# Performance work log

Measured on AMD Instinct MI355X. Metric: run time of the kernel, lower is better.

The kernel has to match this reference:

```python
import jax, jax.numpy as jnp
import numpy as np

CHUNK_SIZE = 256


def setup_inputs() -> dict:
    key = jax.random.key(0)
    kq, kk, kv = jax.random.split(key, 3)
    b, h, L, d, dv = 2, 16, 4096, 16, 64
    return {
        "q": jax.random.normal(kq, (b, h, L, d), dtype=jnp.float32),
        "k": jax.random.normal(kk, (b, h, L, d), dtype=jnp.float32),
        "v": jax.random.normal(kv, (b, h, L, dv), dtype=jnp.float32),
    }


def reference(q, k, v):
    b, h, L, d = q.shape
    dv = v.shape[-1]
    cs = CHUNK_SIZE
    n = L // cs

    q = q * d ** (-0.5)

    # ---- normalizer z over full sequence ----
    k_cumsum = jnp.cumsum(k, axis=-2)                               # [b,h,L,d]
    kk_cumsum = jnp.cumsum(k[..., :, None] * k[..., None, :], axis=-3)  # [b,h,L,d,d]
    z = (q * k_cumsum).sum(-1)
    z = z + 0.5 * jnp.einsum('bhld,bhle,bhlde->bhl', q, q, kk_cumsum)
    z = z + (jnp.arange(L, dtype=z.dtype) + 1.0)[None, None, :]

    # ---- zeroth-order term ----
    o_const = jnp.cumsum(v, axis=-2)                                # [b,h,L,dv]

    # ---- chunked view ----
    qc = q.reshape(b, h, n, cs, d)
    kc = k.reshape(b, h, n, cs, d)
    vc = v.reshape(b, h, n, cs, dv)

    # intra-chunk quadratic attention: S + 0.5*S^2, causal-masked
    s = jnp.einsum('bhnqd,bhnkd->bhnqk', qc, kc)                    # [b,h,n,cs,cs]
    s = s + 0.5 * s ** 2
    causal_mask = jnp.tril(jnp.ones((cs, cs), dtype=bool))
    s = jnp.where(causal_mask, s, jnp.zeros((), dtype=s.dtype))
    o = jnp.einsum('bhnqk,bhnkf->bhnqf', s, vc)                     # [b,h,n,cs,dv]

    # inter-chunk quadratic state: cumulative K x K x V from previous chunks
    kv_quad = jnp.einsum('bhncd,bhnce,bhncf->bhndef', kc, kc, vc)   # [b,h,n,d,d,dv]
    kv_quad = jnp.cumsum(kv_quad, axis=2)
    kv_quad = jnp.concatenate(
        [jnp.zeros_like(kv_quad[:, :, :1]), kv_quad[:, :, :-1]], axis=2)
    o = o + 0.5 * jnp.einsum('bhndef,bhncd,bhnce->bhncf', kv_quad, qc, qc)

    # inter-chunk linear state: cumulative K x V from previous chunks
    kv_lin = jnp.einsum('bhncd,bhnce->bhnde', kc, vc)               # [b,h,n,d,dv]
    kv_lin = jnp.cumsum(kv_lin, axis=2)
    kv_lin = jnp.concatenate(
        [jnp.zeros_like(kv_lin[:, :, :1]), kv_lin[:, :, :-1]], axis=2)
    o = o + jnp.einsum('bhnde,bhncd->bhnce', kv_lin, qc)

    o = o.reshape(b, h, L, dv) + o_const
    return o / (z[..., None] + 1e-6)
```

## Files before the change

kernel.cpp:

```cpp
#include <hip/hip_runtime.h>
#include <hip/hip_cooperative_groups.h>
#include <cstddef>

#define BH    32
#define LSEQ  4096
#define D     16
#define DV    64
#define CS    256
#define NC    16
#define NF    160
#define NZ    65
#define KSTEPS 5
#define PER   (NZ * NF)
#define QXS   20

typedef short short8 __attribute__((ext_vector_type(8)));
typedef float f32x4 __attribute__((ext_vector_type(4)));
typedef float f4 __attribute__((ext_vector_type(4)));
typedef unsigned uint4v __attribute__((ext_vector_type(4)));

#define OFF_KBF 0u
#define OFF_VT  (4u*1024u*1024u)
#define OFF_ST  (OFF_VT + (unsigned)(BH*NZ*LSEQ*2))

__device__ __forceinline__ unsigned f2bf(float x) {
  unsigned u = __float_as_uint(x);
  return (u + 0x7FFFu + ((u >> 16) & 1u)) >> 16;
}
__device__ __forceinline__ float bf2f(unsigned short u) {
  return __uint_as_float(((unsigned)u) << 16);
}
__device__ __forceinline__ short8 zero8() {
  short8 z = {0,0,0,0,0,0,0,0};
  return z;
}
__device__ __forceinline__ unsigned cvtpk(float lo, float hi) {
  unsigned r;
  asm("v_cvt_pk_bf16_f32 %0, %1, %2" : "=v"(r) : "v"(lo), "v"(hi));
  return r;
}
__device__ __forceinline__ short8 pk4(unsigned a, unsigned b, unsigned c, unsigned d) {
  uint4v u = {a, b, c, d};
  return __builtin_bit_cast(short8, u);
}

__device__ __forceinline__ unsigned feat_tbl(int f) {
  if (f == 0)  return 16u | (16u << 8);
  if (f <= 16) return (unsigned)(f - 1) | (16u << 8);
  if (f < 137) {
    int p = f - 17, off = 0;
    for (int d = 0; d < 15; ++d) {
      int cnt = 15 - d;
      if (p < off + cnt) return (unsigned)d | ((unsigned)(d + 1 + p - off) << 8);
      off += cnt;
    }
  }
  if (f < 153) {
    int d = f - 137;
    return (unsigned)d | ((unsigned)d << 8) | (1u << 16);
  }
  return 17u | (17u << 8);
}

struct Smem {
  float kxqx[CS][QXS];
  __align__(16) unsigned short vt[NZ][264];
  union {
    __align__(16) unsigned short stt[NZ][168];
    struct {
      __align__(16) unsigned short ptile[8][1280];
      float zline[CS];
    } u;
  } b;
  unsigned tbl[NF];
};

__global__ __launch_bounds__(512, 4) void unified(const float* __restrict__ q,
                                                  const float* __restrict__ k,
                                                  const float* __restrict__ v,
                                                  unsigned* __restrict__ kbf_u32,
                                                  unsigned short* __restrict__ st,
                                                  float* __restrict__ out) {
  __shared__ Smem sm;
  int blk = blockIdx.x, bh = blk >> 4, c = blk & 15;
  int t = threadIdx.x, w = t >> 6, lane = t & 63, quad = lane >> 4, n16 = lane & 15;
  const size_t base = (size_t)bh * LSEQ + (size_t)c * CS;

  {
    const f4* K4 = (const f4*)(k + base * D);
    uint2* kbd2 = (uint2*)(kbf_u32 + base * D / 2);
    for (int idx = t; idx < 1024; idx += 512) {
      f4 kv = K4[idx];
      kbd2[idx] = make_uint2(cvtpk(kv[0], kv[1]), cvtpk(kv[2], kv[3]));
      *(f4*)&sm.kxqx[idx >> 2][(idx & 3) * 4] = kv;
    }
    for (int i = t; i < CS; i += 512)
      *(float2*)&sm.kxqx[i][16] = make_float2(1.f, 0.f);
    const f4* V4 = (const f4*)(v + base * DV);
    for (int idx = t; idx < 2048; idx += 512) {
      int m16 = idx & 15, j0 = (idx >> 4) * 2;
      f4 a  = V4[j0 * 16 + m16];
      f4 bq = V4[j0 * 16 + 16 + m16];
#pragma unroll
      for (int r = 0; r < 4; ++r)
        *(unsigned*)&sm.vt[m16 * 4 + r][j0] = cvtpk(a[r], bq[r]);
    }
    if (t < 128) ((unsigned*)&sm.vt[64][0])[t] = 0x3F803F80u;
    if (t < NF) sm.tbl[t] = feat_tbl(t);
  }
  __syncthreads();

  if (c < 15 && w < 5) {
    unsigned tv0 = sm.tbl[(w * 2 + 0) * 16 + n16];
    unsigned tv1 = sm.tbl[(w * 2 + 1) * 16 + n16];
    int d0 = tv0 & 255, e0 = (tv0 >> 8) & 255;
    int d1 = tv1 & 255, e1 = (tv1 >> 8) & 255;
    f32x4 acc[2][5];
#pragma unroll
    for (int mm = 0; mm < 2; ++mm)
#pragma unroll
      for (int nt = 0; nt < 5; ++nt) acc[mm][nt] = (f32x4){0.f, 0.f, 0.f, 0.f};
    for (int jt = 0; jt < 8; ++jt) {
      float x0[8], x1[8];
#pragma unroll
      for (int i = 0; i < 8; ++i) {
        const float* kr = &sm.kxqx[jt * 32 + quad * 8 + i][0];
        x0[i] = kr[d0] * kr[e0];
        x1[i] = kr[d1] * kr[e1];
      }
      short8 afr0 = pk4(cvtpk(x0[0], x0[1]), cvtpk(x0[2], x0[3]),
                        cvtpk(x0[4], x0[5]), cvtpk(x0[6], x0[7]));
      short8 afr1 = pk4(cvtpk(x1[0], x1[1]), cvtpk(x1[2], x1[3]),
                        cvtpk(x1[4], x1[5]), cvtpk(x1[6], x1[7]));
      __builtin_amdgcn_s_setprio(1);
#pragma unroll
      for (int nt = 0; nt < 5; ++nt) {
        int ncol = nt * 16 + n16;
        short8 b = zero8();
        if (ncol < NZ) b = *(const short8*)(&sm.vt[ncol][jt * 32 + quad * 8]);
        acc[0][nt] = __builtin_amdgcn_mfma_f32_16x16x32_bf16(afr0, b, acc[0][nt], 0, 0, 0);
        acc[1][nt] = __builtin_amdgcn_mfma_f32_16x16x32_bf16(afr1, b, acc[1][nt], 0, 0, 0);
      }
      __builtin_amdgcn_s_setprio(0);
    }
    unsigned short* stc = st + (size_t)(bh * NC + c) * PER;
#pragma unroll
    for (int mm = 0; mm < 2; ++mm) {
      int feat0 = (w * 2 + mm) * 16 + quad * 4;
      float sc[4];
#pragma unroll
      for (int r = 0; r < 4; ++r)
        sc[r] = (feat0 + r >= 137 && feat0 + r < 153) ? 0.5f : 1.0f;
#pragma unroll
      for (int nt = 0; nt < 5; ++nt) {
        int col = nt * 16 + n16;
        if (col < NZ) {
          unsigned lo = cvtpk(acc[mm][nt][0] * sc[0], acc[mm][nt][1] * sc[1]);
          unsigned hi = cvtpk(acc[mm][nt][2] * sc[2], acc[mm][nt][3] * sc[3]);
          *(uint2*)(stc + (size_t)col * NF + feat0) = make_uint2(lo, hi);
        }
      }
    }
  }
  __syncthreads();

  {
    const f4* Q4 = (const f4*)(q + base * D);
    for (int idx = t; idx < 1024; idx += 512) {
      f4 qv = Q4[idx] * 0.25f;
      *(f4*)&sm.kxqx[idx >> 2][(idx & 3) * 4] = qv;
    }
  }

  cooperative_groups::this_grid().sync();

  if (c > 0) {
    const unsigned short* stg = st + (size_t)bh * NC * PER;
    float s0[8], s1[8], s2[8];
#pragma unroll
    for (int e = 0; e < 8; ++e) { s0[e] = 0.f; s1[e] = 0.f; s2[e] = 0.f; }
    const int i0 = t * 8, i1 = i0 + 4096, i2 = i0 + 8192;
    const bool h2 = (i2 < PER);
    for (int cc = 0; cc < c; ++cc) {
      const unsigned short* pcc = stg + (size_t)cc * PER;
      short8 a0 = *(const short8*)(pcc + i0);
      short8 a1 = *(const short8*)(pcc + i1);
      short8 a2 = h2 ? *(const short8*)(pcc + i2) : zero8();
#pragma unroll
      for (int e = 0; e < 8; ++e) {
        s0[e] += bf2f((unsigned short)a0[e]);
        s1[e] += bf2f((unsigned short)a1[e]);
        s2[e] += bf2f((unsigned short)a2[e]);
      }
    }
    {
      int col = i0 / NF, ft = i0 - col * NF;
      *(short8*)(&sm.b.stt[col][ft]) =
          pk4(cvtpk(s0[0], s0[1]), cvtpk(s0[2], s0[3]),
              cvtpk(s0[4], s0[5]), cvtpk(s0[6], s0[7]));
      col = i1 / NF; ft = i1 - col * NF;
      *(short8*)(&sm.b.stt[col][ft]) =
          pk4(cvtpk(s1[0], s1[1]), cvtpk(s1[2], s1[3]),
              cvtpk(s1[4], s1[5]), cvtpk(s1[6], s1[7]));
      if (h2) {
        col = i2 / NF; ft = i2 - col * NF;
        *(short8*)(&sm.b.stt[col][ft]) =
            pk4(cvtpk(s2[0], s2[1]), cvtpk(s2[2], s2[3]),
                cvtpk(s2[4], s2[5]), cvtpk(s2[6], s2[7]));
      }
    }
  }
  __syncthreads();

  f32x4 acc[2][5];
#pragma unroll
  for (int mm = 0; mm < 2; ++mm)
#pragma unroll
    for (int nt = 0; nt < 5; ++nt) acc[mm][nt] = (f32x4){0.f, 0.f, 0.f, 0.f};

  if (c > 0) {
    const float* qrow0 = &sm.kxqx[(w * 2 + 0) * 16 + n16][0];
    const float* qrow1 = &sm.kxqx[(w * 2 + 1) * 16 + n16][0];
    for (int ks = 0; ks < KSTEPS; ++ks) {
      unsigned tvv[8];
#pragma unroll
      for (int i = 0; i < 8; ++i) tvv[i] = sm.tbl[ks * 32 + quad * 8 + i];
      float x0[8], x1[8];
#pragma unroll
      for (int i = 0; i < 8; ++i) {
        int d = tvv[i] & 255, e = (tvv[i] >> 8) & 255;
        x0[i] = qrow0[d] * qrow0[e];
        x1[i] = qrow1[d] * qrow1[e];
      }
      short8 afr0 = pk4(cvtpk(x0[0], x0[1]), cvtpk(x0[2], x0[3]),
                        cvtpk(x0[4], x0[5]), cvtpk(x0[6], x0[7]));
      short8 afr1 = pk4(cvtpk(x1[0], x1[1]), cvtpk(x1[2], x1[3]),
                        cvtpk(x1[4], x1[5]), cvtpk(x1[6], x1[7]));
      __builtin_amdgcn_s_setprio(1);
#pragma unroll
      for (int nt = 0; nt < 5; ++nt) {
        int ncol = nt * 16 + n16;
        short8 b = zero8();
        if (ncol < NZ) b = *(const short8*)(&sm.b.stt[ncol][ks * 32 + quad * 8]);
        acc[0][nt] = __builtin_amdgcn_mfma_f32_16x16x32_bf16(afr0, b, acc[0][nt], 0, 0, 0);
        acc[1][nt] = __builtin_amdgcn_mfma_f32_16x16x32_bf16(afr1, b, acc[1][nt], 0, 0, 0);
      }
      __builtin_amdgcn_s_setprio(0);
    }
  }
  __syncthreads();

  short8 qfr[2];
#pragma unroll
  for (int mm = 0; mm < 2; ++mm) {
    int m = (w * 2 + mm) * 16 + n16;
    short8 a = zero8();
    if (quad < 2) {
      const float* qr = &sm.kxqx[m][quad * 8];
      f4 q0 = *(const f4*)(qr);
      f4 q1 = *(const f4*)(qr + 4);
      a = pk4(cvtpk(q0[0], q0[1]), cvtpk(q0[2], q0[3]),
              cvtpk(q1[0], q1[1]), cvtpk(q1[2], q1[3]));
    }
    qfr[mm] = a;
  }
  const unsigned short* kbc = (const unsigned short*)kbf_u32 + base * D;
  unsigned short* pw = &sm.b.u.ptile[w][0];
  short8 ones;
#pragma unroll
  for (int i = 0; i < 8; ++i) ones[i] = (short)0x3F80;

  for (int jt = 0; jt <= w; ++jt) {
    short8 kb[2];
#pragma unroll
    for (int ntk = 0; ntk < 2; ++ntk) {
      short8 b = zero8();
      if (quad < 2)
        b = *(const short8*)(kbc + (size_t)(jt * 32 + ntk * 16 + n16) * D + quad * 8);
      kb[ntk] = b;
    }
    f32x4 zf = (f32x4){0.f, 0.f, 0.f, 0.f};
    f32x4 s[2][2];
    __builtin_amdgcn_s_setprio(1);
#pragma unroll
    for (int mm = 0; mm < 2; ++mm)
#pragma unroll
      for (int ntk = 0; ntk < 2; ++ntk)
        s[mm][ntk] = __builtin_amdgcn_mfma_f32_16x16x32_bf16(qfr[mm], kb[ntk], zf, 0, 0, 0);
    __builtin_amdgcn_s_setprio(0);
    bool diag = (jt == w);
#pragma unroll
    for (int mm = 0; mm < 2; ++mm)
#pragma unroll
      for (int ntk = 0; ntk < 2; ++ntk) {
        float ph[4];
#pragma unroll
        for (int r = 0; r < 4; ++r) {
          float sv = s[mm][ntk][r];
          float phi = fmaf(sv, fmaf(0.5f, sv, 1.0f), 1.0f);
          if (diag) {
            int qrow = mm * 16 + quad * 4 + r;
            int kcol = ntk * 16 + n16;
            if (kcol > qrow) phi = 0.f;
          }
          ph[r] = phi;
        }
        unsigned u01 = cvtpk(ph[0], ph[1]);
        unsigned u23 = cvtpk(ph[2], ph[3]);
        int rb = (mm * 16 + quad * 4) * 40 + ntk * 16 + n16;
        pw[rb      ] = (unsigned short)u01;
        pw[rb +  40] = (unsigned short)(u01 >> 16);
        pw[rb +  80] = (unsigned short)u23;
        pw[rb + 120] = (unsigned short)(u23 >> 16);
      }
    short8 pa[2];
#pragma unroll
    for (int mm = 0; mm < 2; ++mm)
      pa[mm] = *(const short8*)(pw + (mm * 16 + n16) * 40 + quad * 8);
    __builtin_amdgcn_s_setprio(1);
#pragma unroll
    for (int nt = 0; nt < 5; ++nt) {
      int ncol = nt * 16 + n16;
      short8 b;
      if (ncol < 64)       b = *(const short8*)(&sm.vt[ncol][jt * 32 + quad * 8]);
      else if (ncol == 64) b = ones;
      else                 b = zero8();
      acc[0][nt] = __builtin_amdgcn_mfma_f32_16x16x32_bf16(pa[0], b, acc[0][nt], 0, 0, 0);
      acc[1][nt] = __builtin_amdgcn_mfma_f32_16x16x32_bf16(pa[1], b, acc[1][nt], 0, 0, 0);
    }
    __builtin_amdgcn_s_setprio(0);
  }

  if (n16 == 0) {
#pragma unroll
    for (int mm = 0; mm < 2; ++mm)
#pragma unroll
      for (int r = 0; r < 4; ++r)
        sm.b.u.zline[(w * 2 + mm) * 16 + quad * 4 + r] = acc[mm][4][r];
  }
  float* oc = out + base * DV;
#pragma unroll
  for (int mm = 0; mm < 2; ++mm)
#pragma unroll
    for (int r = 0; r < 4; ++r) {
      int qrow = (w * 2 + mm) * 16 + quad * 4 + r;
      float inv = __builtin_amdgcn_rcpf(sm.b.u.zline[qrow] + 1e-6f);
#pragma unroll
      for (int nt = 0; nt < 4; ++nt)
        oc[(size_t)qrow * DV + nt * 16 + n16] = acc[mm][nt][r] * inv;
    }
}

__global__ __launch_bounds__(320) void pass_a(const float* __restrict__ k,
                                              const float* __restrict__ v,
                                              unsigned* __restrict__ kbf_u32,
                                              unsigned* __restrict__ vt_u32,
                                              unsigned short* __restrict__ st) {
  __shared__ float kx[CS][18];
  __shared__ __align__(16) unsigned short vt_lds[NZ][264];
  __shared__ unsigned tbl[NF];
  int blk = blockIdx.x, bh = blk >> 4, c = blk & 15;
  int t = threadIdx.x, w = t >> 6, lane = t & 63, quad = lane >> 4, n16 = lane & 15;
  {
    const float2* kc2 = (const float2*)(k + ((size_t)bh * LSEQ + c * CS) * D);
    unsigned* kbd = kbf_u32 + ((size_t)bh * LSEQ + c * CS) * D / 2;
    for (int i = t; i < 2048; i += 320) {
      float2 v2 = kc2[i];
      kbd[i] = f2bf(v2.x) | (f2bf(v2.y) << 16);
      int j = i >> 3, dd = (i & 7) * 2;
      kx[j][dd] = v2.x; kx[j][dd + 1] = v2.y;
    }
    for (int i = t; i < CS; i += 320) { kx[i][16] = 1.f; kx[i][17] = 0.f; }
  }
  {
    const float* vb = v + ((size_t)bh * LSEQ + c * CS) * DV;
    for (int i = t; i < CS * DV; i += 320) {
      int j = i >> 6, f = i & 63;
      vt_lds[f][j] = (unsigned short)f2bf(vb[i]);
    }
    for (int i = t; i < CS; i += 320) vt_lds[64][i] = (unsigned short)0x3F80;
  }
  if (t < NF) tbl[t] = feat_tbl(t);
  __syncthreads();
  {
    unsigned* vtg = vt_u32 + (size_t)bh * NZ * (LSEQ / 2) + c * (CS / 2);
    for (int i = t; i < NZ * (CS / 2); i += 320) {
      int f = i >> 7, jp = (i & 127) * 2;
      vtg[(size_t)f * (LSEQ / 2) + (i & 127)] =
          (unsigned)vt_lds[f][jp] | ((unsigned)vt_lds[f][jp + 1] << 16);
    }
  }
  f32x4 acc[2][5];
#pragma unroll
  for (int mm = 0; mm < 2; ++mm)
#pragma unroll
    for (int nt = 0; nt < 5; ++nt) acc[mm][nt] = (f32x4){0.f, 0.f, 0.f, 0.f};
  for (int jt = 0; jt < 8; ++jt) {
    short8 afr[2];
#pragma unroll
    for (int mm = 0; mm < 2; ++mm) {
      int feat = (w * 2 + mm) * 16 + n16;
      unsigned tv = tbl[feat];
      int d = tv & 255, e = (tv >> 8) & 255;
      short8 a;
#pragma unroll
      for (int i = 0; i < 8; ++i) {
        int jj = jt * 32 + quad * 8 + i;
        a[i] = (short)f2bf(kx[jj][d] * kx[jj][e]);
      }
      afr[mm] = a;
    }
#pragma unroll
    for (int nt = 0; nt < 5; ++nt) {
      int ncol = nt * 16 + n16;
      short8 b = zero8();
      if (ncol < NZ) b = *(const short8*)(&vt_lds[ncol][jt * 32 + quad * 8]);
      acc[0][nt] = __builtin_amdgcn_mfma_f32_16x16x32_bf16(afr[0], b, acc[0][nt], 0, 0, 0);
      acc[1][nt] = __builtin_amdgcn_mfma_f32_16x16x32_bf16(afr[1], b, acc[1][nt], 0, 0, 0);
    }
  }
  unsigned short* stc = st + (size_t)(bh * NC + c) * PER;
#pragma unroll
  for (int mm = 0; mm < 2; ++mm)
#pragma unroll
    for (int nt = 0; nt < 5; ++nt) {
      int col = nt * 16 + n16;
      if (col < NZ) {
        unsigned lo = f2bf(acc[mm][nt][0]) | (f2bf(acc[mm][nt][1]) << 16);
        unsigned hi = f2bf(acc[mm][nt][2]) | (f2bf(acc[mm][nt][3]) << 16);
        int feat0 = (w * 2 + mm) * 16 + quad * 4;
        *(uint2*)(stc + (size_t)col * NF + feat0) = make_uint2(lo, hi);
      }
    }
}

__global__ __launch_bounds__(256) void pass_b(unsigned short* __restrict__ st) {
  const int TOT = BH * PER;
  int idx = blockIdx.x * 256 + threadIdx.x;
  if (idx >= TOT) return;
  int bh = idx / PER, r = idx - bh * PER;
  unsigned short* p = st + (size_t)bh * NC * PER + r;
  float run = 0.f;
#pragma unroll
  for (int c = 0; c < NC; ++c) {
    unsigned short uv = p[(size_t)c * PER];
    float val = bf2f(uv);
    p[(size_t)c * PER] = (unsigned short)f2bf(run);
    run += val;
  }
}

__global__ __launch_bounds__(512) void pass_c(const float* __restrict__ q,
                                              const unsigned short* __restrict__ kbf,
                                              const unsigned short* __restrict__ vt,
                                              const unsigned short* __restrict__ st,
                                              float* __restrict__ out) {
  __shared__ float qx[CS][18];
  __shared__ unsigned tbl[NF];
  __shared__ __align__(16) unsigned short ptile[8][32 * 40];
  __shared__ float zline[CS];
  int blk = blockIdx.x, bh = blk >> 4, c = blk & 15;
  const size_t base = (size_t)bh * LSEQ + (size_t)c * CS;
  const float* qc = q + base * D;
  int t = threadIdx.x, w = t >> 6, lane = t & 63, quad = lane >> 4, n16 = lane & 15;
  for (int i = t; i < CS * D; i += 512) {
    int row = i >> 4, dd = i & 15;
    qx[row][dd] = qc[i] * 0.25f;
  }
  for (int i = t; i < CS; i += 512) { qx[i][16] = 1.f; qx[i][17] = 0.f; }
  if (t < NF) tbl[t] = feat_tbl(t);
  __syncthreads();
  f32x4 acc[2][5];
#pragma unroll
  for (int mm = 0; mm < 2; ++mm)
#pragma unroll
    for (int nt = 0; nt < 5; ++nt) acc[mm][nt] = (f32x4){0.f, 0.f, 0.f, 0.f};
  if (c > 0) {
    const unsigned short* stc = st + (size_t)(bh * NC + c) * PER;
    for (int ks = 0; ks < KSTEPS; ++ks) {
      short8 afr[2];
#pragma unroll
      for (int mm = 0; mm < 2; ++mm) {
        const float* qrow = qx[(w * 2 + mm) * 16 + n16];
        short8 a;
#pragma unroll
        for (int i = 0; i < 8; ++i) {
          int f = ks * 32 + quad * 8 + i;
          unsigned tv = tbl[f];
          float val = qrow[tv & 255] * qrow[(tv >> 8) & 255];
          if (tv & 0x10000u) val *= 0.5f;
          a[i] = (short)f2bf(val);
        }
        afr[mm] = a;
      }
#pragma unroll
      for (int nt = 0; nt < 5; ++nt) {
        int ncol = nt * 16 + n16;
        short8 b = zero8();
        if (ncol < NZ) b = *(const short8*)(stc + (size_t)ncol * NF + ks * 32 + quad * 8);
        acc[0][nt] = __builtin_amdgcn_mfma_f32_16x16x32_bf16(afr[0], b, acc[0][nt], 0, 0, 0);
        acc[1][nt] = __builtin_amdgcn_mfma_f32_16x16x32_bf16(afr[1], b, acc[1][nt], 0, 0, 0);
      }
    }
  }
  short8 qfr[2];
#pragma unroll
  for (int mm = 0; mm < 2; ++mm) {
    int m = (w * 2 + mm) * 16 + n16;
    short8 a = zero8();
    if (quad < 2) {
#pragma unroll
      for (int i = 0; i < 8; ++i) a[i] = (short)f2bf(qx[m][quad * 8 + i]);
    }
    qfr[mm] = a;
  }
  const unsigned short* kbc = kbf + base * D;
  const unsigned short* vtb = vt + (size_t)bh * NZ * LSEQ + (size_t)c * CS;
  unsigned short* pw = &ptile[w][0];
  short8 ones;
#pragma unroll
  for (int i = 0; i < 8; ++i) ones[i] = (short)0x3F80;
  for (int jt = 0; jt <= w; ++jt) {
    short8 kb[2];
#pragma unroll
    for (int ntk = 0; ntk < 2; ++ntk) {
      short8 b = zero8();
      if (quad < 2)
        b = *(const short8*)(kbc + (size_t)(jt * 32 + ntk * 16 + n16) * D + quad * 8);
      kb[ntk] = b;
    }
    f32x4 zf = (f32x4){0.f, 0.f, 0.f, 0.f};
    f32x4 s[2][2];
#pragma unroll
    for (int mm = 0; mm < 2; ++mm)
#pragma unroll
      for (int ntk = 0; ntk < 2; ++ntk)
        s[mm][ntk] = __builtin_amdgcn_mfma_f32_16x16x32_bf16(qfr[mm], kb[ntk], zf, 0, 0, 0);
    bool diag = (jt == w);
#pragma unroll
    for (int mm = 0; mm < 2; ++mm)
#pragma unroll
      for (int ntk = 0; ntk < 2; ++ntk)
#pragma unroll
        for (int r = 0; r < 4; ++r) {
          float sv = s[mm][ntk][r];
          float phi = fmaf(0.5f * sv, sv, sv) + 1.0f;
          if (diag) {
            int qrow = mm * 16 + quad * 4 + r;
            int kcol = ntk * 16 + n16;
            if (kcol > qrow) phi = 0.f;
          }
          pw[(mm * 16 + quad * 4 + r) * 40 + ntk * 16 + n16] = (unsigned short)f2bf(phi);
        }
    short8 pa[2];
#pragma unroll
    for (int mm = 0; mm < 2; ++mm)
      pa[mm] = *(const short8*)(pw + (mm * 16 + n16) * 40 + quad * 8);
#pragma unroll
    for (int nt = 0; nt < 5; ++nt) {
      int ncol = nt * 16 + n16;
      short8 b;
      if (ncol < 64)       b = *(const short8*)(vtb + (size_t)ncol * LSEQ + jt * 32 + quad * 8);
      else if (ncol == 64) b = ones;
      else                 b = zero8();
      acc[0][nt] = __builtin_amdgcn_mfma_f32_16x16x32_bf16(pa[0], b, acc[0][nt], 0, 0, 0);
      acc[1][nt] = __builtin_amdgcn_mfma_f32_16x16x32_bf16(pa[1], b, acc[1][nt], 0, 0, 0);
    }
  }
  if (n16 == 0) {
#pragma unroll
    for (int mm = 0; mm < 2; ++mm)
#pragma unroll
      for (int r = 0; r < 4; ++r)
        zline[(w * 2 + mm) * 16 + quad * 4 + r] = acc[mm][4][r];
  }
  float* oc = out + base * DV;
#pragma unroll
  for (int mm = 0; mm < 2; ++mm)
#pragma unroll
    for (int r = 0; r < 4; ++r) {
      int qrow = (w * 2 + mm) * 16 + quad * 4 + r;
      float inv = 1.0f / (zline[qrow] + 1e-6f);
#pragma unroll
      for (int nt = 0; nt < 4; ++nt)
        oc[(size_t)qrow * DV + nt * 16 + n16] = acc[mm][nt][r] * inv;
    }
}

extern "C" void kernel_launch(void* const* d_in, const int* in_sizes, int n_in,
                              void* d_out, int out_size, void* d_ws, size_t ws_size,
                              hipStream_t stream) {
  (void)in_sizes; (void)n_in; (void)out_size; (void)ws_size;
  const float* q = (const float*)d_in[0];
  const float* k = (const float*)d_in[1];
  const float* v = (const float*)d_in[2];
  float* out = (float*)d_out;
  char* wsb = (char*)d_ws;
  unsigned*       kbf32 = (unsigned*)(wsb + OFF_KBF);
  unsigned short* kbf   = (unsigned short*)(wsb + OFF_KBF);
  unsigned*       vt32  = (unsigned*)(wsb + OFF_VT);
  unsigned short* vtp   = (unsigned short*)(wsb + OFF_VT);
  unsigned short* stp   = (unsigned short*)(wsb + OFF_ST);

  int nb = 0;
  hipError_t oe = hipOccupancyMaxActiveBlocksPerMultiprocessor(
      &nb, reinterpret_cast<const void*>(unified), 512, 0);
  if (oe == hipSuccess && nb >= 2) {
    void* args[] = {(void*)&q, (void*)&k, (void*)&v,
                    (void*)&kbf32, (void*)&stp, (void*)&out};
    hipLaunchCooperativeKernel(reinterpret_cast<const void*>(unified),
                               dim3(BH * NC), dim3(512), args, 0, stream);
  } else {
    pass_a<<<BH * NC, 320, 0, stream>>>(k, v, kbf32, vt32, stp);
    pass_b<<<1300, 256, 0, stream>>>(stp);
    pass_c<<<BH * NC, 512, 0, stream>>>(q, kbf, vtp, stp, out);
  }
}
```

Before: 135.2 us.

## Balance causal intra-chunk work by pairing row strips w and 15-w per wave

The intra-chunk causal attention now gives each wave two 16-row strips, w and 15-w, instead of two adjacent strips. Each strip is processed separately, stopping at the last needed 32-key tile, so every wave does a similar amount of work and the triangular mask is skipped more finely. This removes the load imbalance where the last wave did eight tiles while the first did one. It also shrinks the per-wave P tile, narrows the kxqx row padding from 20 to 18 floats with float2 stores, and drops the s_setprio hints. The cost is fewer MFMAs issued per B-fragment load, since each loaded V fragment now feeds one MFMA instead of two.

```diff
diff --git a/kernel.cpp b/kernel.cpp
--- a/kernel.cpp
+++ b/kernel.cpp
@@ -12,7 +12,6 @@
 #define NZ    65
 #define KSTEPS 5
 #define PER   (NZ * NF)
-#define QXS   20
 
 typedef short short8 __attribute__((ext_vector_type(8)));
 typedef float f32x4 __attribute__((ext_vector_type(4)));
@@ -63,12 +62,12 @@
 }
 
 struct Smem {
-  float kxqx[CS][QXS];
+  float kxqx[CS][18];
   __align__(16) unsigned short vt[NZ][264];
   union {
     __align__(16) unsigned short stt[NZ][168];
     struct {
-      __align__(16) unsigned short ptile[8][1280];
+      __align__(16) unsigned short ptile[8][640];
       float zline[CS];
     } u;
   } b;
@@ -92,7 +91,9 @@
     for (int idx = t; idx < 1024; idx += 512) {
       f4 kv = K4[idx];
       kbd2[idx] = make_uint2(cvtpk(kv[0], kv[1]), cvtpk(kv[2], kv[3]));
-      *(f4*)&sm.kxqx[idx >> 2][(idx & 3) * 4] = kv;
+      float* dst = &sm.kxqx[idx >> 2][(idx & 3) * 4];
+      *(float2*)dst = make_float2(kv[0], kv[1]);
+      *(float2*)(dst + 2) = make_float2(kv[2], kv[3]);
     }
     for (int i = t; i < CS; i += 512)
       *(float2*)&sm.kxqx[i][16] = make_float2(1.f, 0.f);
@@ -132,7 +133,6 @@
                         cvtpk(x0[4], x0[5]), cvtpk(x0[6], x0[7]));
       short8 afr1 = pk4(cvtpk(x1[0], x1[1]), cvtpk(x1[2], x1[3]),
                         cvtpk(x1[4], x1[5]), cvtpk(x1[6], x1[7]));
-      __builtin_amdgcn_s_setprio(1);
 #pragma unroll
       for (int nt = 0; nt < 5; ++nt) {
         int ncol = nt * 16 + n16;
@@ -141,7 +141,6 @@
         acc[0][nt] = __builtin_amdgcn_mfma_f32_16x16x32_bf16(afr0, b, acc[0][nt], 0, 0, 0);
         acc[1][nt] = __builtin_amdgcn_mfma_f32_16x16x32_bf16(afr1, b, acc[1][nt], 0, 0, 0);
       }
-      __builtin_amdgcn_s_setprio(0);
     }
     unsigned short* stc = st + (size_t)(bh * NC + c) * PER;
 #pragma unroll
@@ -168,7 +167,9 @@
     const f4* Q4 = (const f4*)(q + base * D);
     for (int idx = t; idx < 1024; idx += 512) {
       f4 qv = Q4[idx] * 0.25f;
-      *(f4*)&sm.kxqx[idx >> 2][(idx & 3) * 4] = qv;
+      float* dst = &sm.kxqx[idx >> 2][(idx & 3) * 4];
+      *(float2*)dst = make_float2(qv[0], qv[1]);
+      *(float2*)(dst + 2) = make_float2(qv[2], qv[3]);
     }
   }
 
@@ -219,8 +220,8 @@
     for (int nt = 0; nt < 5; ++nt) acc[mm][nt] = (f32x4){0.f, 0.f, 0.f, 0.f};
 
   if (c > 0) {
-    const float* qrow0 = &sm.kxqx[(w * 2 + 0) * 16 + n16][0];
-    const float* qrow1 = &sm.kxqx[(w * 2 + 1) * 16 + n16][0];
+    const float* qrow0 = &sm.kxqx[w * 16 + n16][0];
+    const float* qrow1 = &sm.kxqx[(15 - w) * 16 + n16][0];
     for (int ks = 0; ks < KSTEPS; ++ks) {
       unsigned tvv[8];
 #pragma unroll
@@ -236,7 +237,6 @@
                         cvtpk(x0[4], x0[5]), cvtpk(x0[6], x0[7]));
       short8 afr1 = pk4(cvtpk(x1[0], x1[1]), cvtpk(x1[2], x1[3]),
                         cvtpk(x1[4], x1[5]), cvtpk(x1[6], x1[7]));
-      __builtin_amdgcn_s_setprio(1);
 #pragma unroll
       for (int nt = 0; nt < 5; ++nt) {
         int ncol = nt * 16 + n16;
@@ -245,110 +245,98 @@
         acc[0][nt] = __builtin_amdgcn_mfma_f32_16x16x32_bf16(afr0, b, acc[0][nt], 0, 0, 0);
         acc[1][nt] = __builtin_amdgcn_mfma_f32_16x16x32_bf16(afr1, b, acc[1][nt], 0, 0, 0);
       }
-      __builtin_amdgcn_s_setprio(0);
     }
   }
   __syncthreads();
 
-  short8 qfr[2];
-#pragma unroll
-  for (int mm = 0; mm < 2; ++mm) {
-    int m = (w * 2 + mm) * 16 + n16;
-    short8 a = zero8();
-    if (quad < 2) {
-      const float* qr = &sm.kxqx[m][quad * 8];
-      f4 q0 = *(const f4*)(qr);
-      f4 q1 = *(const f4*)(qr + 4);
-      a = pk4(cvtpk(q0[0], q0[1]), cvtpk(q0[2], q0[3]),
-              cvtpk(q1[0], q1[1]), cvtpk(q1[2], q1[3]));
-    }
-    qfr[mm] = a;
-  }
   const unsigned short* kbc = (const unsigned short*)kbf_u32 + base * D;
   unsigned short* pw = &sm.b.u.ptile[w][0];
   short8 ones;
 #pragma unroll
   for (int i = 0; i < 8; ++i) ones[i] = (short)0x3F80;
 
-  for (int jt = 0; jt <= w; ++jt) {
-    short8 kb[2];
-#pragma unroll
-    for (int ntk = 0; ntk < 2; ++ntk) {
-      short8 b = zero8();
-      if (quad < 2)
-        b = *(const short8*)(kbc + (size_t)(jt * 32 + ntk * 16 + n16) * D + quad * 8);
-      kb[ntk] = b;
-    }
-    f32x4 zf = (f32x4){0.f, 0.f, 0.f, 0.f};
-    f32x4 s[2][2];
-    __builtin_amdgcn_s_setprio(1);
-#pragma unroll
-    for (int mm = 0; mm < 2; ++mm)
-#pragma unroll
-      for (int ntk = 0; ntk < 2; ++ntk)
-        s[mm][ntk] = __builtin_amdgcn_mfma_f32_16x16x32_bf16(qfr[mm], kb[ntk], zf, 0, 0, 0);
-    __builtin_amdgcn_s_setprio(0);
-    bool diag = (jt == w);
-#pragma unroll
-    for (int mm = 0; mm < 2; ++mm)
+#pragma unroll
+  for (int mm = 0; mm < 2; ++mm) {
+    const int s = mm ? (15 - w) : w;
+    short8 qf = zero8();
+    if (quad < 2) {
+      const float2* qr = (const float2*)&sm.kxqx[s * 16 + n16][quad * 8];
+      float2 q0 = qr[0], q1 = qr[1], q2 = qr[2], q3 = qr[3];
+      qf = pk4(cvtpk(q0.x, q0.y), cvtpk(q1.x, q1.y),
+               cvtpk(q2.x, q2.y), cvtpk(q3.x, q3.y));
+    }
+    const int ntiles = (s >> 1) + 1;
+    for (int jt = 0; jt < ntiles; ++jt) {
+      short8 kb[2];
+#pragma unroll
+      for (int ntk = 0; ntk < 2; ++ntk) {
+        short8 b = zero8();
+        if (quad < 2)
+          b = *(const short8*)(kbc + (size_t)(jt * 32 + ntk * 16 + n16) * D + quad * 8);
+        kb[ntk] = b;
+      }
+      f32x4 zf = (f32x4){0.f, 0.f, 0.f, 0.f};
+      f32x4 sres[2];
+      sres[0] = __builtin_amdgcn_mfma_f32_16x16x32_bf16(qf, kb[0], zf, 0, 0, 0);
+      sres[1] = __builtin_amdgcn_mfma_f32_16x16x32_bf16(qf, kb[1], zf, 0, 0, 0);
+      const bool last = (jt == ntiles - 1);
 #pragma unroll
       for (int ntk = 0; ntk < 2; ++ntk) {
         float ph[4];
 #pragma unroll
         for (int r = 0; r < 4; ++r) {
-          float sv = s[mm][ntk][r];
+          float sv = sres[ntk][r];
           float phi = fmaf(sv, fmaf(0.5f, sv, 1.0f), 1.0f);
-          if (diag) {
-            int qrow = mm * 16 + quad * 4 + r;
-            int kcol = ntk * 16 + n16;
-            if (kcol > qrow) phi = 0.f;
+          if (last) {
+            int qrow_g = s * 16 + quad * 4 + r;
+            int kcol_g = jt * 32 + ntk * 16 + n16;
+            if (kcol_g > qrow_g) phi = 0.f;
           }
           ph[r] = phi;
         }
         unsigned u01 = cvtpk(ph[0], ph[1]);
         unsigned u23 = cvtpk(ph[2], ph[3]);
-        int rb = (mm * 16 + quad * 4) * 40 + ntk * 16 + n16;
+        int rb = (quad * 4) * 40 + ntk * 16 + n16;
         pw[rb      ] = (unsigned short)u01;
         pw[rb +  40] = (unsigned short)(u01 >> 16);
         pw[rb +  80] = (unsigned short)u23;
         pw[rb + 120] = (unsigned short)(u23 >> 16);
       }
-    short8 pa[2];
-#pragma unroll
-    for (int mm = 0; mm < 2; ++mm)
-      pa[mm] = *(const short8*)(pw + (mm * 16 + n16) * 40 + quad * 8);
-    __builtin_amdgcn_s_setprio(1);
-#pragma unroll
-    for (int nt = 0; nt < 5; ++nt) {
-      int ncol = nt * 16 + n16;
-      short8 b;
-      if (ncol < 64)       b = *(const short8*)(&sm.vt[ncol][jt * 32 + quad * 8]);
-      else if (ncol == 64) b = ones;
-      else                 b = zero8();
-      acc[0][nt] = __builtin_amdgcn_mfma_f32_16x16x32_bf16(pa[0], b, acc[0][nt], 0, 0, 0);
-      acc[1][nt] = __builtin_amdgcn_mfma_f32_16x16x32_bf16(pa[1], b, acc[1][nt], 0, 0, 0);
-    }
-    __builtin_amdgcn_s_setprio(0);
+      short8 pa = *(const short8*)(pw + n16 * 40 + quad * 8);
+#pragma unroll
+      for (int nt = 0; nt < 5; ++nt) {
+        int ncol = nt * 16 + n16;
+        short8 b;
+        if (ncol < 64)       b = *(const short8*)(&sm.vt[ncol][jt * 32 + quad * 8]);
+        else if (ncol == 64) b = ones;
+        else                 b = zero8();
+        acc[mm][nt] = __builtin_amdgcn_mfma_f32_16x16x32_bf16(pa, b, acc[mm][nt], 0, 0, 0);
+      }
+    }
   }
 
   if (n16 == 0) {
 #pragma unroll
-    for (int mm = 0; mm < 2; ++mm)
+    for (int mm = 0; mm < 2; ++mm) {
+      int s = mm ? (15 - w) : w;
 #pragma unroll
       for (int r = 0; r < 4; ++r)
-        sm.b.u.zline[(w * 2 + mm) * 16 + quad * 4 + r] = acc[mm][4][r];
+        sm.b.u.zline[s * 16 + quad * 4 + r] = acc[mm][4][r];
+    }
   }
   float* oc = out + base * DV;
 #pragma unroll
-  for (int mm = 0; mm < 2; ++mm)
+  for (int mm = 0; mm < 2; ++mm) {
+    int s = mm ? (15 - w) : w;
 #pragma unroll
     for (int r = 0; r < 4; ++r) {
-      int qrow = (w * 2 + mm) * 16 + quad * 4 + r;
+      int qrow = s * 16 + quad * 4 + r;
       float inv = __builtin_amdgcn_rcpf(sm.b.u.zline[qrow] + 1e-6f);
 #pragma unroll
       for (int nt = 0; nt < 4; ++nt)
         oc[(size_t)qrow * DV + nt * 16 + n16] = acc[mm][nt][r] * inv;
     }
+  }
 }
 
 __global__ __launch_bounds__(320) void pass_a(const float* __restrict__ k,
```

After: 135.2 us. About the same (+0.0%).
